# Optimization experiments

Measured on AMD Instinct MI355X. Metric: run time of the kernel, lower is better.

The kernel has to match this reference:

```python
import jax, jax.numpy as jnp
import numpy as np

VOCAB = 21
EPS = 1e-5


def rmsnorm(x, w):
    return x * jax.lax.rsqrt(jnp.mean(x * x, axis=-1, keepdims=True) + EPS) * w


def mamba_layer(h, in_w, conv_w, conv_b, xp_w, dtp_w, dtp_b, A_log, Dp, out_w):
    # h: (B, L, D)
    Bsz, L, _ = h.shape
    di, dc = conv_w.shape
    n = A_log.shape[-1]
    r = dtp_w.shape[-1]
    xz = jnp.einsum('bld,ed->ble', h, in_w)          # (B, L, 2*di)
    xi, z = jnp.split(xz, 2, axis=-1)
    # causal depthwise conv of width dc
    xp = jnp.pad(xi, ((0, 0), (dc - 1, 0), (0, 0)))
    xc = conv_b + sum(xp[:, k:k + L, :] * conv_w[:, k] for k in range(dc))
    xc = jax.nn.silu(xc)                              # (B, L, di)
    dbc = jnp.einsum('bld,ed->ble', xc, xp_w)         # (B, L, r+2n)
    dt, Bm, Cm = dbc[..., :r], dbc[..., r:r + n], dbc[..., r + n:]
    dt = jax.nn.softplus(jnp.einsum('blr,dr->bld', dt, dtp_w) + dtp_b)  # (B, L, di)
    A = -jnp.exp(A_log)                               # (di, n)

    def step(hst, inp):
        x_t, dt_t, B_t, C_t = inp                     # (B,di),(B,di),(B,n),(B,n)
        dA = jnp.exp(dt_t[..., None] * A)             # (B, di, n)
        hst = dA * hst + (dt_t * x_t)[..., None] * B_t[:, None, :]
        y_t = jnp.einsum('bdn,bn->bd', hst, C_t)
        return hst, y_t

    h0 = jnp.zeros((Bsz, di, n), dtype=h.dtype)
    xs = (xc.swapaxes(0, 1), dt.swapaxes(0, 1), Bm.swapaxes(0, 1), Cm.swapaxes(0, 1))
    _, ys = jax.lax.scan(step, h0, xs)
    y = ys.swapaxes(0, 1) + xc * Dp                   # skip term D*x
    y = y * jax.nn.silu(z)                            # gate
    return jnp.einsum('bld,ed->ble', y, out_w)


def setup_inputs() -> dict:
    key = jax.random.key(0)
    B, L, D = 4, 1024, 512
    n_layers, n, dc, expand = 2, 16, 3, 2
    di = expand * D
    r = (D + 15) // 16  # dt_rank = ceil(d_model/16) = 32
    ks = jax.random.split(key, 12)
    f32 = jnp.float32
    inp = {}
    inp['x'] = jax.random.randint(ks[0], (B, L), 0, VOCAB)
    inp['emb'] = 0.02 * jax.random.normal(ks[1], (VOCAB, D), f32)
    inp['norm_w'] = jnp.ones((n_layers, D), f32)
    inp['in_proj_w'] = (D ** -0.5) * jax.random.normal(ks[2], (n_layers, 2 * di, D), f32)
    inp['conv_w'] = (dc ** -0.5) * jax.random.normal(ks[3], (n_layers, di, dc), f32)
    inp['conv_b'] = jnp.zeros((n_layers, di), f32)
    inp['x_proj_w'] = (di ** -0.5) * jax.random.normal(ks[4], (n_layers, r + 2 * n, di), f32)
    inp['dt_proj_w'] = (r ** -0.5) * jax.random.normal(ks[5], (n_layers, di, r), f32)
    inp['dt_proj_b'] = jax.random.uniform(ks[6], (n_layers, di), f32, minval=-4.0, maxval=-1.0)
    inp['A_log'] = jnp.log(jnp.broadcast_to(jnp.arange(1, n + 1, dtype=f32), (n_layers, di, n)))
    inp['D_param'] = jnp.ones((n_layers, di), f32)
    inp['out_proj_w'] = (di ** -0.5) * jax.random.normal(ks[7], (n_layers, D, di), f32)
    inp['fc_w'] = (D ** -0.5) * jax.random.normal(ks[8], (2, D), f32)
    inp['fc_b'] = jnp.zeros((2,), f32)
    return inp


def reference(x, emb, norm_w, in_proj_w, conv_w, conv_b, x_proj_w, dt_proj_w,
              dt_proj_b, A_log, D_param, out_proj_w, fc_w, fc_b):
    h = emb[x].astype(jnp.float32)                    # (B, L, D)
    n_layers = norm_w.shape[0]
    for l in range(n_layers):
        h = rmsnorm(
            mamba_layer(h, in_proj_w[l], conv_w[l], conv_b[l], x_proj_w[l],
                        dt_proj_w[l], dt_proj_b[l], A_log[l], D_param[l],
                        out_proj_w[l]),
            norm_w[l])
    pooled = jnp.mean(h, axis=1)                      # global_pool=True
    out = jnp.tanh(pooled)                            # dropout is identity at eval
    return out @ fc_w.T + fc_b                        # (B, 2)
```

## Files before the change

### kernel.cpp

```cpp
#include <hip/hip_runtime.h>
#include <math.h>

constexpr int Bsz = 4, Lseq = 1024, Dmodel = 512, NLAYERS = 2;
constexpr int DI = 1024, NST = 16, RNK = 32;
constexpr int BLQ = Bsz * Lseq;
constexpr int NCH = 32, CLEN = 32;

typedef __attribute__((ext_vector_type(8))) short short8v;
typedef __attribute__((ext_vector_type(8))) unsigned short ushort8v;
typedef __attribute__((ext_vector_type(4))) float f32x4;
typedef unsigned short ushort;

__device__ inline ushort bf16_rne(float v) {
  unsigned u = __float_as_uint(v);
  u += 0x7FFFu + ((u >> 16) & 1u);
  return (ushort)(u >> 16);
}
__device__ inline float bf2f(ushort u) {
  return __uint_as_float(((unsigned)u) << 16);
}
__device__ inline size_t frag_off(int row, int k, int KT) {
  int kt = k >> 6, kk = (k >> 5) & 1, k8 = (k >> 3) & 3;
  int lanei = (row & 15) | (k8 << 4), msub = (row >> 4) & 7, rt = row >> 7;
  return ((((size_t)(rt * KT + kt) * 2 + kk) * 8 + msub) * 64 + lanei) * 8;
}
#define GLDS(gp, lp) __builtin_amdgcn_global_load_lds( \
    (const __attribute__((address_space(1))) void*)(gp), \
    (__attribute__((address_space(3))) void*)(lp), 16, 0, 0)

__global__ __launch_bounds__(256) void embed_kernel(const int* __restrict__ x,
    const float* __restrict__ emb, ushort* __restrict__ Af) {
  int i = blockIdx.x * 256 + threadIdx.x;
  int row = i >> 6, k = (i & 63) * 8;
  int tok = x[row];
  const float* src = &emb[(size_t)tok * Dmodel + k];
  float4 v0 = *reinterpret_cast<const float4*>(src);
  float4 v1 = *reinterpret_cast<const float4*>(src + 4);
  float xs[8] = {v0.x, v0.y, v0.z, v0.w, v1.x, v1.y, v1.z, v1.w};
  ushort hv[8];
#pragma unroll
  for (int e = 0; e < 8; ++e) hv[e] = bf16_rne(xs[e]);
  *reinterpret_cast<ushort8v*>(&Af[frag_off(row, k, 8)]) =
      *reinterpret_cast<ushort8v*>(hv);
}

__global__ __launch_bounds__(256) void cvtw_kernel(
    const float* __restrict__ in_w, const float* __restrict__ xp_w,
    const float* __restrict__ out_w,
    ushort* __restrict__ WIh, ushort* __restrict__ WIl,
    ushort* __restrict__ XPh, ushort* __restrict__ XPl,
    ushort* __restrict__ WOh, ushort* __restrict__ WOl)
{
  int blk = blockIdx.x;
  const float* src; ushort *dh, *dl; size_t doff;
  if (blk < 1024) {
    int u = blk * 256 + threadIdx.x;
    int l = u >> 17, rem = u & 131071;
    int row = rem >> 6, k = (rem & 63) * 8;
    src = in_w + (size_t)l * 2048 * 512 + (size_t)row * 512 + k;
    size_t base = (size_t)l * 2048 * 512;
    dh = WIh + base; dl = WIl + base; doff = frag_off(row, k, 8);
  } else if (blk < 1088) {
    int u = (blk - 1024) * 256 + threadIdx.x;
    int l = u >> 13, rem = u & 8191;
    int row = rem >> 7, k = (rem & 127) * 8;
    src = xp_w + (size_t)l * 64 * 1024 + (size_t)row * 1024 + k;
    size_t base = (size_t)l * 131072;
    dh = XPh + base; dl = XPl + base; doff = frag_off(row, k, 16);
  } else {
    int u = (blk - 1088) * 256 + threadIdx.x;
    int l = u >> 16, rem = u & 65535;
    int row = rem >> 7, k = (rem & 127) * 8;
    src = out_w + (size_t)l * 512 * 1024 + (size_t)row * 1024 + k;
    size_t base = (size_t)l * 512 * 1024;
    dh = WOh + base; dl = WOl + base; doff = frag_off(row, k, 16);
  }
  float4 v0 = *reinterpret_cast<const float4*>(src);
  float4 v1 = *reinterpret_cast<const float4*>(src + 4);
  float xs[8] = {v0.x, v0.y, v0.z, v0.w, v1.x, v1.y, v1.z, v1.w};
  ushort hs[8], ls[8];
#pragma unroll
  for (int j = 0; j < 8; ++j) {
    unsigned u = __float_as_uint(xs[j]);
    float hf = __uint_as_float(u & 0xFFFF0000u);
    float r = xs[j] - hf;
    hs[j] = (ushort)(u >> 16);
    ls[j] = (ushort)(__float_as_uint(r) >> 16);
  }
  *reinterpret_cast<ushort8v*>(&dh[doff]) = *reinterpret_cast<ushort8v*>(hs);
  *reinterpret_cast<ushort8v*>(&dl[doff]) = *reinterpret_cast<ushort8v*>(ls);
}

template<int OB, int SPLITB>
__global__ __launch_bounds__(256) void gemm_mfma(
    const ushort* __restrict__ Ah,
    const ushort* __restrict__ Bh, const ushort* __restrict__ Bl,
    void* __restrict__ Cv, int N, int K)
{
  const int KT = K >> 6;
  constexpr int ASZ = 2 * 8 * 64 * 8;
  __shared__ ushort lds[3 * ASZ];
  const int tid = threadIdx.x;
  const int lane = tid & 63, wid = tid >> 6;
  const int wm = wid >> 1, wn = wid & 1;
  const int bm0 = blockIdx.y * 128, bn0 = blockIdx.x * 128;
  const size_t abase = (size_t)blockIdx.y * KT * ASZ;
  const size_t bbase = (size_t)blockIdx.x * KT * ASZ;
  const ushort* gsrc = (wid == 0) ? Ah : (wid == 1) ? Bh : Bl;
  const size_t gb = (wid == 0) ? abase : bbase;
  f32x4 acc[4][4];
#pragma unroll
  for (int i = 0; i < 4; ++i)
#pragma unroll
    for (int j = 0; j < 4; ++j) acc[i][j] = (f32x4){0.f, 0.f, 0.f, 0.f};
  const int msel = wm * 4, nsel = wn * 4;
  for (int kt = 0; kt < KT; ++kt) {
    if (wid < (SPLITB ? 3 : 2)) {
      const ushort* sbase = gsrc + gb + (size_t)kt * ASZ + lane * 8;
#pragma unroll
      for (int i = 0; i < 16; ++i)
        GLDS(sbase + i * 512, lds + wid * ASZ + i * 512);
    }
    __syncthreads();
#pragma unroll
    for (int kk = 0; kk < 2; ++kk) {
      short8v a_h[4], b_h[4], b_l[4];
#pragma unroll
      for (int i = 0; i < 4; ++i) {
        int ai = ((kk * 8 + msel + i) * 64 + lane) * 8;
        int bi = ((kk * 8 + nsel + i) * 64 + lane) * 8;
        a_h[i] = *reinterpret_cast<const short8v*>(&lds[0 * ASZ + ai]);
        b_h[i] = *reinterpret_cast<const short8v*>(&lds[1 * ASZ + bi]);
        if (SPLITB) b_l[i] = *reinterpret_cast<const short8v*>(&lds[2 * ASZ + bi]);
      }
#pragma unroll
      for (int ms = 0; ms < 4; ++ms)
#pragma unroll
        for (int ns = 0; ns < 4; ++ns) {
          acc[ms][ns] = __builtin_amdgcn_mfma_f32_16x16x32_bf16(a_h[ms], b_h[ns], acc[ms][ns], 0, 0, 0);
          if (SPLITB)
            acc[ms][ns] = __builtin_amdgcn_mfma_f32_16x16x32_bf16(a_h[ms], b_l[ns], acc[ms][ns], 0, 0, 0);
        }
    }
    __syncthreads();
  }
  const int cr = lane >> 4, cc = lane & 15;
#pragma unroll
  for (int ms = 0; ms < 4; ++ms) {
    int row0 = bm0 + (msel + ms) * 16 + cr * 4;
#pragma unroll
    for (int ns = 0; ns < 4; ++ns) {
      int col = bn0 + (nsel + ns) * 16 + cc;
#pragma unroll
      for (int r = 0; r < 4; ++r) {
        if (OB) ((ushort*)Cv)[(size_t)(row0 + r) * N + col] = bf16_rne(acc[ms][ns][r]);
        else    ((float*)Cv)[(size_t)(row0 + r) * N + col] = acc[ms][ns][r];
      }
    }
  }
}

__global__ __launch_bounds__(256) void convxp_kernel(
    const ushort* __restrict__ XZb, const float* __restrict__ cw,
    const float* __restrict__ cb,
    const ushort* __restrict__ XPh, const ushort* __restrict__ XPl,
    float* __restrict__ XC, float* __restrict__ P)
{
  constexpr int XZOFF = 0;
  constexpr int AOFF  = 1312;
  constexpr int BHOFF = 2336;
  constexpr int BLOFF = 6432;
  __shared__ ushort smu[10528];
  const int tid = threadIdx.x, lane = tid & 63, wid = tid >> 6;
  const int cr = lane >> 4, cc = lane & 15;
  const int bm0 = blockIdx.x * 16;
  const int z = blockIdx.y;
  const int batchbase = bm0 & ~(Lseq - 1);
  f32x4 acc = (f32x4){0.f, 0.f, 0.f, 0.f};

  for (int kt = z * 8; kt < z * 8 + 8; ++kt) {
    const int kcol0 = kt * 64;
    if (wid < 2) {
#pragma unroll
      for (int i = 0; i < 2; ++i) {
        int u = tid + i * 128;
        if (u < 144) {
          int r = u >> 3, c8 = u & 7;
          int grow = bm0 - 2 + r;
          ushort8v v = {};
          if (grow >= batchbase)
            v = *reinterpret_cast<const ushort8v*>(
                &XZb[(size_t)grow * 2048 + kcol0 + c8 * 8]);
          *reinterpret_cast<ushort8v*>(&smu[XZOFF + r * 72 + c8 * 8]) = v;
        }
      }
    } else {
      const ushort* src = ((wid == 2) ? XPh : XPl) + (size_t)kt * 8192 + lane * 8;
      int dst0 = (wid == 2) ? BHOFF : BLOFF;
#pragma unroll
      for (int i = 0; i < 8; ++i) {
        int sidx = (i >> 2) * 8 + (i & 3);
        GLDS(src + sidx * 512, smu + dst0 + i * 512);
      }
    }
    __syncthreads();
    if (tid < 128) {
      int row = tid >> 3, c8 = tid & 7;
      int d0 = kcol0 + c8 * 8;
      ushort8v cur = *reinterpret_cast<ushort8v*>(&smu[XZOFF + (row + 2) * 72 + c8 * 8]);
      ushort8v pm1 = *reinterpret_cast<ushort8v*>(&smu[XZOFF + (row + 1) * 72 + c8 * 8]);
      ushort8v pm2 = *reinterpret_cast<ushort8v*>(&smu[XZOFF + (row + 0) * 72 + c8 * 8]);
      float wv[24], bv[8];
#pragma unroll
      for (int q = 0; q < 6; ++q)
        *reinterpret_cast<float4*>(&wv[q * 4]) =
            *reinterpret_cast<const float4*>(&cw[d0 * 3 + q * 4]);
      *reinterpret_cast<float4*>(&bv[0]) = *reinterpret_cast<const float4*>(&cb[d0]);
      *reinterpret_cast<float4*>(&bv[4]) = *reinterpret_cast<const float4*>(&cb[d0 + 4]);
      float os[8]; ushort hv[8];
#pragma unroll
      for (int e = 0; e < 8; ++e) {
        float a = bv[e];
        a = fmaf(bf2f(pm2[e]), wv[e * 3 + 0], a);
        a = fmaf(bf2f(pm1[e]), wv[e * 3 + 1], a);
        a = fmaf(bf2f(cur[e]), wv[e * 3 + 2], a);
        float s = a / (1.f + __expf(-a));
        os[e] = s; hv[e] = bf16_rne(s);
      }
      float* op = &XC[(size_t)(bm0 + row) * DI + d0];
      *reinterpret_cast<float4*>(op) = *reinterpret_cast<float4*>(&os[0]);
      *reinterpret_cast<float4*>(op + 4) = *reinterpret_cast<float4*>(&os[4]);
      int kk = c8 >> 2, k8 = c8 & 3;
      int idx = (kk * 64 + (row | (k8 << 4))) ^ k8;
      *reinterpret_cast<ushort8v*>(&smu[AOFF + idx * 8]) =
          *reinterpret_cast<ushort8v*>(hv);
    }
    __syncthreads();
#pragma unroll
    for (int kk = 0; kk < 2; ++kk) {
      int aidx = (kk * 64 + lane) ^ ((lane >> 4) & 3);
      short8v a = *reinterpret_cast<const short8v*>(&smu[AOFF + aidx * 8]);
      short8v bh = *reinterpret_cast<const short8v*>(&smu[BHOFF + ((kk * 4 + wid) * 64 + lane) * 8]);
      short8v bl = *reinterpret_cast<const short8v*>(&smu[BLOFF + ((kk * 4 + wid) * 64 + lane) * 8]);
      acc = __builtin_amdgcn_mfma_f32_16x16x32_bf16(a, bh, acc, 0, 0, 0);
      acc = __builtin_amdgcn_mfma_f32_16x16x32_bf16(a, bl, acc, 0, 0, 0);
    }
    __syncthreads();
  }
  float* Pz = P + (size_t)z * BLQ * 64;
#pragma unroll
  for (int r = 0; r < 4; ++r)
    Pz[(size_t)(bm0 + cr * 4 + r) * 64 + wid * 16 + cc] = acc[r];
}

__global__ __launch_bounds__(256) void xpost_kernel(
    const float* __restrict__ P, const float* __restrict__ dtw,
    const float* __restrict__ dtb, float* __restrict__ DTb,
    float* __restrict__ BCc)
{
  const int tid = threadIdx.x;
  const size_t SL = (size_t)BLQ * 64;
  if (blockIdx.y == 16) {
    int i0 = blockIdx.x * 4096 + tid;
#pragma unroll
    for (int i = 0; i < 16; ++i) {
      int idx = i0 + i * 256;
      int bt = idx >> 5, n = idx & 31;
      size_t g = (size_t)bt * 64 + 32 + n;
      BCc[idx] = P[g] + P[SL + g];
    }
    return;
  }
  const int dg = blockIdx.y, bm0 = blockIdx.x * 128;
  __shared__ float db[128][33];
  __shared__ float wt[64][33];
#pragma unroll
  for (int i = 0; i < 16; ++i) {
    int e = tid + i * 256;
    int r = e >> 5, c = e & 31;
    size_t g = (size_t)(bm0 + r) * 64 + c;
    db[r][c] = P[g] + P[SL + g];
  }
#pragma unroll
  for (int i = 0; i < 8; ++i) {
    int e = tid + i * 256;
    int r = e >> 5, c = e & 31;
    wt[r][c] = dtw[(size_t)(dg * 64 + r) * 32 + c];
  }
  __syncthreads();
  const int d_loc = tid & 63, wv = tid >> 6;
  const float bias = dtb[dg * 64 + d_loc];
#pragma unroll 4
  for (int i = 0; i < 32; ++i) {
    int r = wv + i * 4;
    float dot = 0.f;
#pragma unroll
    for (int c = 0; c < 32; ++c) dot = fmaf(db[r][c], wt[d_loc][c], dot);
    float v = dot + bias;
    DTb[(size_t)(bm0 + r) * DI + dg * 64 + d_loc] =
        (v > 15.f) ? v : log1pf(__expf(v));
  }
}

__global__ __launch_bounds__(256) void scan_p1_kernel(
    const float* __restrict__ DTb, const float* __restrict__ XC,
    const float* __restrict__ BCc, const float* __restrict__ Alog,
    float* __restrict__ HEND, float* __restrict__ DSUM)
{
  const int d = blockIdx.x * 256 + threadIdx.x;
  const int c = blockIdx.y, b = blockIdx.z;
  const int t0 = b * Lseq + c * CLEN;
  __shared__ float Bs[CLEN][16];
#pragma unroll
  for (int i = 0; i < 2; ++i) {
    int e = threadIdx.x + i * 256;
    Bs[e >> 4][e & 15] = BCc[(size_t)(t0 + (e >> 4)) * 32 + (e & 15)];
  }
  float An[16];
#pragma unroll
  for (int j = 0; j < 4; ++j) {
    float4 a = *reinterpret_cast<const float4*>(&Alog[d * 16 + j * 4]);
    An[j * 4 + 0] = -__expf(a.x); An[j * 4 + 1] = -__expf(a.y);
    An[j * 4 + 2] = -__expf(a.z); An[j * 4 + 3] = -__expf(a.w);
  }
  __syncthreads();
  float h[16] = {};
  float S = 0.f;
  for (int t = 0; t < CLEN; ++t) {
    size_t g = (size_t)(t0 + t) * DI + d;
    float dt = DTb[g], xc = XC[g];
    S += dt;
    float dtxc = dt * xc;
#pragma unroll
    for (int n = 0; n < 16; ++n)
      h[n] = fmaf(__expf(An[n] * dt), h[n], dtxc * Bs[t][n]);
  }
  size_t hb = ((size_t)(b * NCH + c) * DI + d) * 16;
#pragma unroll
  for (int j = 0; j < 4; ++j)
    *reinterpret_cast<float4*>(&HEND[hb + j * 4]) =
        *reinterpret_cast<float4*>(&h[j * 4]);
  DSUM[(size_t)(b * NCH + c) * DI + d] = S;
}

__global__ __launch_bounds__(256) void scan_p2_kernel(
    float* __restrict__ HEND, const float* __restrict__ DSUM,
    const float* __restrict__ Alog)
{
  int id = blockIdx.x * 256 + threadIdx.x;
  int n = id & 15, d = (id >> 4) & (DI - 1), b = id >> 14;
  float An = -__expf(Alog[d * 16 + n]);
  float hg = 0.f;
  for (int c = 0; c < NCH; ++c) {
    size_t hi = ((size_t)(b * NCH + c) * DI + d) * 16 + n;
    float hl = HEND[hi];
    float Dc = DSUM[(size_t)(b * NCH + c) * DI + d];
    HEND[hi] = hg;
    hg = fmaf(__expf(An * Dc), hg, hl);
  }
}

__global__ __launch_bounds__(256) void scan_p3_kernel(
    const float* __restrict__ XC, const float* __restrict__ DTb,
    const float* __restrict__ BCc, const ushort* __restrict__ XZb,
    const float* __restrict__ HEND, const float* __restrict__ Alog,
    const float* __restrict__ Dp, ushort* __restrict__ Af)
{
  const int tid = threadIdx.x;
  const int dg = blockIdx.x, c = blockIdx.y, b = blockIdx.z;
  const int d = dg * 256 + tid;
  const int t0 = b * Lseq + c * CLEN;
  __shared__ float BC[CLEN][32];
  __shared__ float ys[CLEN][264];
#pragma unroll
  for (int i = 0; i < 4; ++i) {
    int e = tid + i * 256;
    BC[e >> 5][e & 31] = BCc[(size_t)(t0 + (e >> 5)) * 32 + (e & 31)];
  }
  float An[16], h[16];
  size_t hb = ((size_t)(b * NCH + c) * DI + d) * 16;
#pragma unroll
  for (int j = 0; j < 4; ++j) {
    float4 a = *reinterpret_cast<const float4*>(&Alog[d * 16 + j * 4]);
    An[j * 4 + 0] = -__expf(a.x); An[j * 4 + 1] = -__expf(a.y);
    An[j * 4 + 2] = -__expf(a.z); An[j * 4 + 3] = -__expf(a.w);
    *reinterpret_cast<float4*>(&h[j * 4]) =
        *reinterpret_cast<const float4*>(&HEND[hb + j * 4]);
  }
  float Dpv = Dp[d];
  __syncthreads();
  for (int t = 0; t < CLEN; ++t) {
    size_t g = (size_t)(t0 + t) * DI + d;
    float dt = DTb[g], xc = XC[g];
    float z = bf2f(XZb[(size_t)(t0 + t) * (2 * DI) + DI + d]);
    float dtxc = dt * xc;
    float y = 0.f;
#pragma unroll
    for (int n = 0; n < 16; ++n) {
      h[n] = fmaf(__expf(An[n] * dt), h[n], dtxc * BC[t][n]);
      y = fmaf(h[n], BC[t][16 + n], y);
    }
    float sil = z / (1.f + __expf(-z));
    ys[t][tid] = (y + xc * Dpv) * sil;
  }
  __syncthreads();
#pragma unroll
  for (int i = 0; i < 4; ++i) {
    int u = tid + i * 256;
    int tt = u >> 5, j8 = u & 31;
    int row = t0 + tt;
    int kg = dg * 256 + j8 * 8;
    ushort hv[8];
#pragma unroll
    for (int e = 0; e < 8; ++e) hv[e] = bf16_rne(ys[tt][j8 * 8 + e]);
    *reinterpret_cast<ushort8v*>(&Af[frag_off(row, kg, 16)]) =
        *reinterpret_cast<ushort8v*>(hv);
  }
}

__global__ __launch_bounds__(256) void rmsnorm_kernel(const float* __restrict__ X,
    const float* __restrict__ W, float* __restrict__ O, ushort* __restrict__ Af) {
  int row = blockIdx.x * 4 + (threadIdx.x >> 6);
  int lane = threadIdx.x & 63;
  int k = lane * 8;
  const float* xp = X + (size_t)row * Dmodel + k;
  float4 v0 = *reinterpret_cast<const float4*>(xp);
  float4 v1 = *reinterpret_cast<const float4*>(xp + 4);
  float vs[8] = {v0.x, v0.y, v0.z, v0.w, v1.x, v1.y, v1.z, v1.w};
  float ss = 0.f;
#pragma unroll
  for (int e = 0; e < 8; ++e) ss = fmaf(vs[e], vs[e], ss);
#pragma unroll
  for (int o = 32; o >= 1; o >>= 1) ss += __shfl_xor(ss, o);
  float sc = rsqrtf(ss * (1.f / Dmodel) + 1e-5f);
  const float* wp = W + k;
  float4 w0 = *reinterpret_cast<const float4*>(wp);
  float4 w1 = *reinterpret_cast<const float4*>(wp + 4);
  float wsv[8] = {w0.x, w0.y, w0.z, w0.w, w1.x, w1.y, w1.z, w1.w};
  float os[8];
  ushort hv[8];
#pragma unroll
  for (int e = 0; e < 8; ++e) {
    os[e] = vs[e] * sc * wsv[e];
    hv[e] = bf16_rne(os[e]);
  }
  float* op = O + (size_t)row * Dmodel + k;
  *reinterpret_cast<float4*>(op) = *reinterpret_cast<float4*>(&os[0]);
  *reinterpret_cast<float4*>(op + 4) = *reinterpret_cast<float4*>(&os[4]);
  *reinterpret_cast<ushort8v*>(&Af[frag_off(row, k, 8)]) =
      *reinterpret_cast<ushort8v*>(hv);
}

__global__ __launch_bounds__(256) void pool_part_kernel(const float* __restrict__ H,
    float* __restrict__ part) {
  int b = blockIdx.x, dg = blockIdx.y, tc = blockIdx.z;
  int tid = threadIdx.x;
  int d = dg * 128 + (tid & 127);
  int ph = tid >> 7;
  const float* base = H + ((size_t)(b * Lseq + tc * 128 + ph * 64)) * Dmodel + d;
  float s = 0.f;
#pragma unroll 8
  for (int t = 0; t < 64; ++t) s += base[(size_t)t * Dmodel];
  __shared__ float red[256];
  red[tid] = s; __syncthreads();
  if (ph == 0)
    part[(size_t)(b * 8 + tc) * Dmodel + d] = red[tid] + red[tid + 128];
}

__global__ __launch_bounds__(256) void pool_head_kernel(
    const float* __restrict__ part, const float* __restrict__ fcw,
    const float* __restrict__ fcb, float* __restrict__ out) {
  int b = blockIdx.x >> 1, j = blockIdx.x & 1;
  int tid = threadIdx.x;
  float s = 0.f;
  for (int d = tid; d < Dmodel; d += 256) {
    float p = 0.f;
#pragma unroll
    for (int tc = 0; tc < 8; ++tc) p += part[(size_t)(b * 8 + tc) * Dmodel + d];
    s += tanhf(p * (1.f / Lseq)) * fcw[j * Dmodel + d];
  }
#pragma unroll
  for (int o = 32; o >= 1; o >>= 1) s += __shfl_xor(s, o);
  __shared__ float w[4];
  if ((tid & 63) == 0) w[tid >> 6] = s;
  __syncthreads();
  if (tid == 0) out[b * 2 + j] = w[0] + w[1] + w[2] + w[3] + fcb[j];
}

extern "C" void kernel_launch(void* const* d_in, const int* in_sizes, int n_in,
                              void* d_out, int out_size, void* d_ws, size_t ws_size,
                              hipStream_t stream) {
  const int*   x      = (const int*)d_in[0];
  const float* emb    = (const float*)d_in[1];
  const float* norm_w = (const float*)d_in[2];
  const float* in_w   = (const float*)d_in[3];
  const float* conv_w = (const float*)d_in[4];
  const float* conv_b = (const float*)d_in[5];
  const float* xp_w   = (const float*)d_in[6];
  const float* dtp_w  = (const float*)d_in[7];
  const float* dtp_b  = (const float*)d_in[8];
  const float* A_log  = (const float*)d_in[9];
  const float* Dp     = (const float*)d_in[10];
  const float* out_w  = (const float*)d_in[11];
  const float* fc_w   = (const float*)d_in[12];
  const float* fc_b   = (const float*)d_in[13];
  float* out = (float*)d_out;

  char* p = (char*)d_ws;
  auto alloc = [&](size_t bytes) { char* r = p; p += (bytes + 255) & ~255ull; return r; };
  ushort* XZb  = (ushort*)alloc((size_t)BLQ * 2 * DI * 2);
  float*  XC   = (float*) alloc((size_t)BLQ * DI * 4);
  float*  DTb  = (float*) alloc((size_t)BLQ * DI * 4);
  float*  BCc  = (float*) alloc((size_t)BLQ * 32 * 4);
  float*  DBCP = (float*) alloc((size_t)2 * BLQ * 64 * 4);
  float*  HEND = (float*) alloc((size_t)Bsz * NCH * DI * 16 * 4);
  float*  DSUM = (float*) alloc((size_t)Bsz * NCH * DI * 4);
  float*  H    = (float*) alloc((size_t)BLQ * Dmodel * 4);
  float*  H2   = (float*) alloc((size_t)BLQ * Dmodel * 4);
  float*  PPART= (float*) alloc((size_t)Bsz * 8 * Dmodel * 4);
  ushort* AhI  = (ushort*)alloc((size_t)BLQ * Dmodel * 2);
  ushort* AhO  = (ushort*)alloc((size_t)BLQ * DI * 2);
  ushort* WIh  = (ushort*)alloc((size_t)2 * 2048 * 512 * 2);
  ushort* WIl  = (ushort*)alloc((size_t)2 * 2048 * 512 * 2);
  ushort* XPh  = (ushort*)alloc((size_t)2 * 131072 * 2);
  ushort* XPl  = (ushort*)alloc((size_t)2 * 131072 * 2);
  ushort* WOh  = (ushort*)alloc((size_t)2 * 512 * 1024 * 2);
  ushort* WOl  = (ushort*)alloc((size_t)2 * 512 * 1024 * 2);

  embed_kernel<<<BLQ * Dmodel / 8 / 256, 256, 0, stream>>>(x, emb, AhI);
  cvtw_kernel<<<1600, 256, 0, stream>>>(in_w, xp_w, out_w,
      WIh, WIl, XPh, XPl, WOh, WOl);

  for (int l = 0; l < NLAYERS; ++l) {
    const float* cw  = conv_w + (size_t)l * DI * 3;
    const float* cb  = conv_b + (size_t)l * DI;
    const float* dtw = dtp_w + (size_t)l * DI * RNK;
    const float* dtb = dtp_b + (size_t)l * DI;
    const float* Al  = A_log + (size_t)l * DI * NST;
    const float* dpl = Dp    + (size_t)l * DI;
    const float* nw  = norm_w + (size_t)l * Dmodel;
    const ushort* wih = WIh + (size_t)l * 2048 * 512;
    const ushort* wil = WIl + (size_t)l * 2048 * 512;
    const ushort* xph = XPh + (size_t)l * 131072;
    const ushort* xpl = XPl + (size_t)l * 131072;
    const ushort* woh = WOh + (size_t)l * 512 * 1024;

    gemm_mfma<1, 1><<<dim3(16, 32), 256, 0, stream>>>(AhI, wih, wil, XZb, 2 * DI, Dmodel);

    convxp_kernel<<<dim3(BLQ / 16, 2), 256, 0, stream>>>(XZb, cw, cb, xph, xpl,
        XC, DBCP);

    xpost_kernel<<<dim3(32, 17), 256, 0, stream>>>(DBCP, dtw, dtb, DTb, BCc);

    scan_p1_kernel<<<dim3(DI / 256, NCH, Bsz), 256, 0, stream>>>(
        DTb, XC, BCc, Al, HEND, DSUM);
    scan_p2_kernel<<<Bsz * DI * NST / 256, 256, 0, stream>>>(HEND, DSUM, Al);
    scan_p3_kernel<<<dim3(DI / 256, NCH, Bsz), 256, 0, stream>>>(
        XC, DTb, BCc, XZb, HEND, Al, dpl, AhO);

    gemm_mfma<0, 0><<<dim3(4, 32), 256, 0, stream>>>(AhO, woh, nullptr, H2, Dmodel, DI);

    rmsnorm_kernel<<<BLQ / 4, 256, 0, stream>>>(H2, nw, H, AhI);
  }

  pool_part_kernel<<<dim3(Bsz, Dmodel / 128, 8), 256, 0, stream>>>(H, PPART);
  pool_head_kernel<<<2 * Bsz, 256, 0, stream>>>(PPART, fc_w, fc_b, out);
}
```

Before: 289.5 us.

## Retile in-proj GEMM, split-K out-proj GEMM, fuse embed and weight conversion

Merges the embedding and weight-conversion kernels into one launch and stops producing the unused low-bf16 half of the out-projection weights. The in-projection GEMM gets a new 64x256 tile using dynamic shared memory. The out-projection GEMM is split over K into two partial outputs, which the rmsnorm kernel now sums as it reads them. The aim is to cut launch count and fill more CUs on the small out-proj GEMM, at the cost of extra partial-sum memory traffic and a large shared-memory footprint in the in-proj kernel.

```diff
diff --git a/kernel.cpp b/kernel.cpp
--- a/kernel.cpp
+++ b/kernel.cpp
@@ -28,52 +28,53 @@
     (const __attribute__((address_space(1))) void*)(gp), \
     (__attribute__((address_space(3))) void*)(lp), 16, 0, 0)
 
-__global__ __launch_bounds__(256) void embed_kernel(const int* __restrict__ x,
-    const float* __restrict__ emb, ushort* __restrict__ Af) {
-  int i = blockIdx.x * 256 + threadIdx.x;
-  int row = i >> 6, k = (i & 63) * 8;
-  int tok = x[row];
-  const float* src = &emb[(size_t)tok * Dmodel + k];
-  float4 v0 = *reinterpret_cast<const float4*>(src);
-  float4 v1 = *reinterpret_cast<const float4*>(src + 4);
-  float xs[8] = {v0.x, v0.y, v0.z, v0.w, v1.x, v1.y, v1.z, v1.w};
-  ushort hv[8];
-#pragma unroll
-  for (int e = 0; e < 8; ++e) hv[e] = bf16_rne(xs[e]);
-  *reinterpret_cast<ushort8v*>(&Af[frag_off(row, k, 8)]) =
-      *reinterpret_cast<ushort8v*>(hv);
-}
-
-__global__ __launch_bounds__(256) void cvtw_kernel(
+__global__ __launch_bounds__(256) void embcvt_kernel(
+    const int* __restrict__ x, const float* __restrict__ emb,
     const float* __restrict__ in_w, const float* __restrict__ xp_w,
     const float* __restrict__ out_w,
+    ushort* __restrict__ Af,
     ushort* __restrict__ WIh, ushort* __restrict__ WIl,
     ushort* __restrict__ XPh, ushort* __restrict__ XPl,
-    ushort* __restrict__ WOh, ushort* __restrict__ WOl)
+    ushort* __restrict__ WOh)
 {
   int blk = blockIdx.x;
-  const float* src; ushort *dh, *dl; size_t doff;
   if (blk < 1024) {
-    int u = blk * 256 + threadIdx.x;
+    int i = blk * 256 + threadIdx.x;
+    int row = i >> 6, k = (i & 63) * 8;
+    int tok = x[row];
+    const float* src = &emb[(size_t)tok * Dmodel + k];
+    float4 v0 = *reinterpret_cast<const float4*>(src);
+    float4 v1 = *reinterpret_cast<const float4*>(src + 4);
+    float xs[8] = {v0.x, v0.y, v0.z, v0.w, v1.x, v1.y, v1.z, v1.w};
+    ushort hv[8];
+#pragma unroll
+    for (int e = 0; e < 8; ++e) hv[e] = bf16_rne(xs[e]);
+    *reinterpret_cast<ushort8v*>(&Af[frag_off(row, k, 8)]) =
+        *reinterpret_cast<ushort8v*>(hv);
+    return;
+  }
+  const float* src; ushort *dh, *dl; size_t doff; bool wantlo = true;
+  if (blk < 2048) {
+    int u = (blk - 1024) * 256 + threadIdx.x;
     int l = u >> 17, rem = u & 131071;
     int row = rem >> 6, k = (rem & 63) * 8;
     src = in_w + (size_t)l * 2048 * 512 + (size_t)row * 512 + k;
     size_t base = (size_t)l * 2048 * 512;
     dh = WIh + base; dl = WIl + base; doff = frag_off(row, k, 8);
-  } else if (blk < 1088) {
-    int u = (blk - 1024) * 256 + threadIdx.x;
+  } else if (blk < 2112) {
+    int u = (blk - 2048) * 256 + threadIdx.x;
     int l = u >> 13, rem = u & 8191;
     int row = rem >> 7, k = (rem & 127) * 8;
     src = xp_w + (size_t)l * 64 * 1024 + (size_t)row * 1024 + k;
     size_t base = (size_t)l * 131072;
     dh = XPh + base; dl = XPl + base; doff = frag_off(row, k, 16);
   } else {
-    int u = (blk - 1088) * 256 + threadIdx.x;
+    int u = (blk - 2112) * 256 + threadIdx.x;
     int l = u >> 16, rem = u & 65535;
     int row = rem >> 7, k = (rem & 127) * 8;
     src = out_w + (size_t)l * 512 * 1024 + (size_t)row * 1024 + k;
     size_t base = (size_t)l * 512 * 1024;
-    dh = WOh + base; dl = WOl + base; doff = frag_off(row, k, 16);
+    dh = WOh + base; dl = nullptr; doff = frag_off(row, k, 16); wantlo = false;
   }
   float4 v0 = *reinterpret_cast<const float4*>(src);
   float4 v1 = *reinterpret_cast<const float4*>(src + 4);
@@ -88,74 +89,152 @@
     ls[j] = (ushort)(__float_as_uint(r) >> 16);
   }
   *reinterpret_cast<ushort8v*>(&dh[doff]) = *reinterpret_cast<ushort8v*>(hs);
-  *reinterpret_cast<ushort8v*>(&dl[doff]) = *reinterpret_cast<ushort8v*>(ls);
-}
-
-template<int OB, int SPLITB>
-__global__ __launch_bounds__(256) void gemm_mfma(
+  if (wantlo)
+    *reinterpret_cast<ushort8v*>(&dl[doff]) = *reinterpret_cast<ushort8v*>(ls);
+}
+
+__global__ __launch_bounds__(256) void gemm_in_mfma(
     const ushort* __restrict__ Ah,
     const ushort* __restrict__ Bh, const ushort* __restrict__ Bl,
-    void* __restrict__ Cv, int N, int K)
-{
-  const int KT = K >> 6;
-  constexpr int ASZ = 2 * 8 * 64 * 8;
-  __shared__ ushort lds[3 * ASZ];
-  const int tid = threadIdx.x;
-  const int lane = tid & 63, wid = tid >> 6;
+    ushort* __restrict__ C)
+{
+  extern __shared__ ushort smu[];
+  constexpr int AOFF = 0, BHOFF = 4096, BLOFF = 20480;
+  const int tid = threadIdx.x, lane = tid & 63, wid = tid >> 6;
+  const int bn = blockIdx.x, bm = blockIdx.y;
+  const int bm0 = bm * 64;
+  const int rtA = bm0 >> 7, half = (bm0 >> 6) & 1;
+  f32x4 acc[4][4];
+#pragma unroll
+  for (int i = 0; i < 4; ++i)
+#pragma unroll
+    for (int j = 0; j < 4; ++j) acc[i][j] = (f32x4){0.f, 0.f, 0.f, 0.f};
+  const int rtB = wid >> 1;
+  const int nsub = (wid & 1) * 4;
+
+  for (int kt = 0; kt < 8; ++kt) {
+    if (wid == 0) {
+      const ushort* cb = Ah + ((size_t)(rtA * 8 + kt)) * 8192;
+#pragma unroll
+      for (int kk = 0; kk < 2; ++kk)
+#pragma unroll
+        for (int m = 0; m < 4; ++m)
+          GLDS(cb + (kk * 8 + half * 4 + m) * 512 + lane * 8,
+               smu + AOFF + (kk * 4 + m) * 512);
+    } else if (wid == 1) {
+#pragma unroll
+      for (int rt = 0; rt < 2; ++rt) {
+        const ushort* cb = Bh + ((size_t)((bn * 2 + rt) * 8 + kt)) * 8192;
+#pragma unroll
+        for (int i = 0; i < 16; ++i)
+          GLDS(cb + i * 512 + lane * 8, smu + BHOFF + rt * 8192 + i * 512);
+      }
+    } else if (wid == 2) {
+#pragma unroll
+      for (int rt = 0; rt < 2; ++rt) {
+        const ushort* cb = Bl + ((size_t)((bn * 2 + rt) * 8 + kt)) * 8192;
+#pragma unroll
+        for (int i = 0; i < 16; ++i)
+          GLDS(cb + i * 512 + lane * 8, smu + BLOFF + rt * 8192 + i * 512);
+      }
+    }
+    __syncthreads();
+#pragma unroll
+    for (int kk = 0; kk < 2; ++kk) {
+      short8v a[4], b[4];
+#pragma unroll
+      for (int i = 0; i < 4; ++i)
+        a[i] = *reinterpret_cast<const short8v*>(&smu[AOFF + ((kk * 4 + i) * 64 + lane) * 8]);
+#pragma unroll
+      for (int j = 0; j < 4; ++j)
+        b[j] = *reinterpret_cast<const short8v*>(
+            &smu[BHOFF + rtB * 8192 + ((kk * 8 + nsub + j) * 64 + lane) * 8]);
+#pragma unroll
+      for (int ms = 0; ms < 4; ++ms)
+#pragma unroll
+        for (int ns = 0; ns < 4; ++ns)
+          acc[ms][ns] = __builtin_amdgcn_mfma_f32_16x16x32_bf16(a[ms], b[ns], acc[ms][ns], 0, 0, 0);
+#pragma unroll
+      for (int j = 0; j < 4; ++j)
+        b[j] = *reinterpret_cast<const short8v*>(
+            &smu[BLOFF + rtB * 8192 + ((kk * 8 + nsub + j) * 64 + lane) * 8]);
+#pragma unroll
+      for (int ms = 0; ms < 4; ++ms)
+#pragma unroll
+        for (int ns = 0; ns < 4; ++ns)
+          acc[ms][ns] = __builtin_amdgcn_mfma_f32_16x16x32_bf16(a[ms], b[ns], acc[ms][ns], 0, 0, 0);
+    }
+    __syncthreads();
+  }
+  const int cr = lane >> 4, cc = lane & 15;
+#pragma unroll
+  for (int ms = 0; ms < 4; ++ms) {
+    int row0 = bm0 + ms * 16 + cr * 4;
+#pragma unroll
+    for (int ns = 0; ns < 4; ++ns) {
+      int col = bn * 256 + wid * 64 + ns * 16 + cc;
+#pragma unroll
+      for (int r = 0; r < 4; ++r)
+        C[(size_t)(row0 + r) * 2048 + col] = bf16_rne(acc[ms][ns][r]);
+    }
+  }
+}
+
+__global__ __launch_bounds__(256) void gemm_out_mfma(
+    const ushort* __restrict__ Ah, const ushort* __restrict__ Bh,
+    float* __restrict__ P)
+{
+  constexpr int ASZ = 8192;
+  __shared__ ushort lds[2 * ASZ];
+  const int tid = threadIdx.x, lane = tid & 63, wid = tid >> 6;
   const int wm = wid >> 1, wn = wid & 1;
-  const int bm0 = blockIdx.y * 128, bn0 = blockIdx.x * 128;
-  const size_t abase = (size_t)blockIdx.y * KT * ASZ;
-  const size_t bbase = (size_t)blockIdx.x * KT * ASZ;
-  const ushort* gsrc = (wid == 0) ? Ah : (wid == 1) ? Bh : Bl;
-  const size_t gb = (wid == 0) ? abase : bbase;
+  const int bm = blockIdx.y, bn = blockIdx.x, z = blockIdx.z;
   f32x4 acc[4][4];
 #pragma unroll
   for (int i = 0; i < 4; ++i)
 #pragma unroll
     for (int j = 0; j < 4; ++j) acc[i][j] = (f32x4){0.f, 0.f, 0.f, 0.f};
   const int msel = wm * 4, nsel = wn * 4;
-  for (int kt = 0; kt < KT; ++kt) {
-    if (wid < (SPLITB ? 3 : 2)) {
-      const ushort* sbase = gsrc + gb + (size_t)kt * ASZ + lane * 8;
+  for (int kt = z * 8; kt < z * 8 + 8; ++kt) {
+    if (wid == 0) {
+      const ushort* cb = Ah + ((size_t)(bm * 16 + kt)) * 8192;
 #pragma unroll
       for (int i = 0; i < 16; ++i)
-        GLDS(sbase + i * 512, lds + wid * ASZ + i * 512);
+        GLDS(cb + i * 512 + lane * 8, lds + i * 512);
+    } else if (wid == 1) {
+      const ushort* cb = Bh + ((size_t)(bn * 16 + kt)) * 8192;
+#pragma unroll
+      for (int i = 0; i < 16; ++i)
+        GLDS(cb + i * 512 + lane * 8, lds + ASZ + i * 512);
     }
     __syncthreads();
 #pragma unroll
     for (int kk = 0; kk < 2; ++kk) {
-      short8v a_h[4], b_h[4], b_l[4];
+      short8v a[4], b[4];
 #pragma unroll
       for (int i = 0; i < 4; ++i) {
-        int ai = ((kk * 8 + msel + i) * 64 + lane) * 8;
-        int bi = ((kk * 8 + nsel + i) * 64 + lane) * 8;
-        a_h[i] = *reinterpret_cast<const short8v*>(&lds[0 * ASZ + ai]);
-        b_h[i] = *reinterpret_cast<const short8v*>(&lds[1 * ASZ + bi]);
-        if (SPLITB) b_l[i] = *reinterpret_cast<const short8v*>(&lds[2 * ASZ + bi]);
+        a[i] = *reinterpret_cast<const short8v*>(&lds[((kk * 8 + msel + i) * 64 + lane) * 8]);
+        b[i] = *reinterpret_cast<const short8v*>(&lds[ASZ + ((kk * 8 + nsel + i) * 64 + lane) * 8]);
       }
 #pragma unroll
       for (int ms = 0; ms < 4; ++ms)
 #pragma unroll
-        for (int ns = 0; ns < 4; ++ns) {
-          acc[ms][ns] = __builtin_amdgcn_mfma_f32_16x16x32_bf16(a_h[ms], b_h[ns], acc[ms][ns], 0, 0, 0);
-          if (SPLITB)
-            acc[ms][ns] = __builtin_amdgcn_mfma_f32_16x16x32_bf16(a_h[ms], b_l[ns], acc[ms][ns], 0, 0, 0);
-        }
+        for (int ns = 0; ns < 4; ++ns)
+          acc[ms][ns] = __builtin_amdgcn_mfma_f32_16x16x32_bf16(a[ms], b[ns], acc[ms][ns], 0, 0, 0);
     }
     __syncthreads();
   }
+  float* Pz = P + (size_t)z * BLQ * Dmodel;
   const int cr = lane >> 4, cc = lane & 15;
 #pragma unroll
   for (int ms = 0; ms < 4; ++ms) {
-    int row0 = bm0 + (msel + ms) * 16 + cr * 4;
+    int row0 = bm * 128 + (msel + ms) * 16 + cr * 4;
 #pragma unroll
     for (int ns = 0; ns < 4; ++ns) {
-      int col = bn0 + (nsel + ns) * 16 + cc;
-#pragma unroll
-      for (int r = 0; r < 4; ++r) {
-        if (OB) ((ushort*)Cv)[(size_t)(row0 + r) * N + col] = bf16_rne(acc[ms][ns][r]);
-        else    ((float*)Cv)[(size_t)(row0 + r) * N + col] = acc[ms][ns][r];
-      }
+      int col = bn * 128 + (nsel + ns) * 16 + cc;
+#pragma unroll
+      for (int r = 0; r < 4; ++r)
+        Pz[(size_t)(row0 + r) * Dmodel + col] = acc[ms][ns][r];
     }
   }
 }
@@ -423,10 +502,14 @@
   int row = blockIdx.x * 4 + (threadIdx.x >> 6);
   int lane = threadIdx.x & 63;
   int k = lane * 8;
-  const float* xp = X + (size_t)row * Dmodel + k;
-  float4 v0 = *reinterpret_cast<const float4*>(xp);
-  float4 v1 = *reinterpret_cast<const float4*>(xp + 4);
-  float vs[8] = {v0.x, v0.y, v0.z, v0.w, v1.x, v1.y, v1.z, v1.w};
+  const size_t SL = (size_t)BLQ * Dmodel;
+  size_t idx = (size_t)row * Dmodel + k;
+  float4 a0 = *reinterpret_cast<const float4*>(&X[idx]);
+  float4 a1 = *reinterpret_cast<const float4*>(&X[idx + 4]);
+  float4 b0 = *reinterpret_cast<const float4*>(&X[SL + idx]);
+  float4 b1 = *reinterpret_cast<const float4*>(&X[SL + idx + 4]);
+  float vs[8] = {a0.x + b0.x, a0.y + b0.y, a0.z + b0.z, a0.w + b0.w,
+                 a1.x + b1.x, a1.y + b1.y, a1.z + b1.z, a1.w + b1.w};
   float ss = 0.f;
 #pragma unroll
   for (int e = 0; e < 8; ++e) ss = fmaf(vs[e], vs[e], ss);
@@ -444,7 +527,7 @@
     os[e] = vs[e] * sc * wsv[e];
     hv[e] = bf16_rne(os[e]);
   }
-  float* op = O + (size_t)row * Dmodel + k;
+  float* op = O + idx;
   *reinterpret_cast<float4*>(op) = *reinterpret_cast<float4*>(&os[0]);
   *reinterpret_cast<float4*>(op + 4) = *reinterpret_cast<float4*>(&os[4]);
   *reinterpret_cast<ushort8v*>(&Af[frag_off(row, k, 8)]) =
@@ -516,7 +599,7 @@
   float*  HEND = (float*) alloc((size_t)Bsz * NCH * DI * 16 * 4);
   float*  DSUM = (float*) alloc((size_t)Bsz * NCH * DI * 4);
   float*  H    = (float*) alloc((size_t)BLQ * Dmodel * 4);
-  float*  H2   = (float*) alloc((size_t)BLQ * Dmodel * 4);
+  float*  H2P  = (float*) alloc((size_t)2 * BLQ * Dmodel * 4);
   float*  PPART= (float*) alloc((size_t)Bsz * 8 * Dmodel * 4);
   ushort* AhI  = (ushort*)alloc((size_t)BLQ * Dmodel * 2);
   ushort* AhO  = (ushort*)alloc((size_t)BLQ * DI * 2);
@@ -525,11 +608,9 @@
   ushort* XPh  = (ushort*)alloc((size_t)2 * 131072 * 2);
   ushort* XPl  = (ushort*)alloc((size_t)2 * 131072 * 2);
   ushort* WOh  = (ushort*)alloc((size_t)2 * 512 * 1024 * 2);
-  ushort* WOl  = (ushort*)alloc((size_t)2 * 512 * 1024 * 2);
-
-  embed_kernel<<<BLQ * Dmodel / 8 / 256, 256, 0, stream>>>(x, emb, AhI);
-  cvtw_kernel<<<1600, 256, 0, stream>>>(in_w, xp_w, out_w,
-      WIh, WIl, XPh, XPl, WOh, WOl);
+
+  embcvt_kernel<<<2624, 256, 0, stream>>>(x, emb, in_w, xp_w, out_w,
+      AhI, WIh, WIl, XPh, XPl, WOh);
 
   for (int l = 0; l < NLAYERS; ++l) {
     const float* cw  = conv_w + (size_t)l * DI * 3;
@@ -545,7 +626,7 @@
     const ushort* xpl = XPl + (size_t)l * 131072;
     const ushort* woh = WOh + (size_t)l * 512 * 1024;
 
-    gemm_mfma<1, 1><<<dim3(16, 32), 256, 0, stream>>>(AhI, wih, wil, XZb, 2 * DI, Dmodel);
+    gemm_in_mfma<<<dim3(8, 64), 256, 73728, stream>>>(AhI, wih, wil, XZb);
 
     convxp_kernel<<<dim3(BLQ / 16, 2), 256, 0, stream>>>(XZb, cw, cb, xph, xpl,
         XC, DBCP);
@@ -558,9 +639,9 @@
     scan_p3_kernel<<<dim3(DI / 256, NCH, Bsz), 256, 0, stream>>>(
         XC, DTb, BCc, XZb, HEND, Al, dpl, AhO);
 
-    gemm_mfma<0, 0><<<dim3(4, 32), 256, 0, stream>>>(AhO, woh, nullptr, H2, Dmodel, DI);
-
-    rmsnorm_kernel<<<BLQ / 4, 256, 0, stream>>>(H2, nw, H, AhI);
+    gemm_out_mfma<<<dim3(4, 32, 2), 256, 0, stream>>>(AhO, woh, H2P);
+
+    rmsnorm_kernel<<<BLQ / 4, 256, 0, stream>>>(H2P, nw, H, AhI);
   }
 
   pool_part_kernel<<<dim3(Bsz, Dmodel / 128, 8), 256, 0, stream>>>(H, PPART);
```

Result: faster. 279.0 us (-3.6%).
